# Kernel tuning notes

Hardware: AMD Instinct MI355X
Metric: run time of the kernel (lower is better)

Reference implementation:

```python
import jax, jax.numpy as jnp
import numpy as np

B, L, D, H = 2, 2048, 1024, 16
HD = D // H
SCALE = HD ** (-0.5)


def setup_inputs() -> dict:
    key = jax.random.key(0)
    ks = jax.random.split(key, 12)
    mk = lambda k, shape: (0.02 * jax.random.normal(k, shape, dtype=jnp.float32))
    return {
        "x_real": jax.random.normal(ks[0], (B, L, D), dtype=jnp.float32),
        "x_imag": jax.random.normal(ks[1], (B, L, D), dtype=jnp.float32),
        "wq_r": mk(ks[2], (D, D)),
        "wq_i": mk(ks[3], (D, D)),
        "wk_r": mk(ks[4], (D, D)),
        "wk_i": mk(ks[5], (D, D)),
        "wv_r": mk(ks[6], (D, D)),
        "wv_i": mk(ks[7], (D, D)),
        "wo_r": mk(ks[8], (D, D)),
        "wo_i": mk(ks[9], (D, D)),
        "bo_r": jnp.zeros((D,), dtype=jnp.float32),
        "bo_i": jnp.zeros((D,), dtype=jnp.float32),
    }


def _clinear(xr, xi, wr, wi):
    # (a+bi)(c+di): real = a@Wr^T - b@Wi^T ; imag = a@Wi^T + b@Wr^T
    r = xr @ wr.T - xi @ wi.T
    i = xr @ wi.T + xi @ wr.T
    return r, i


def _heads(t):
    # [B,L,D] -> [B,H,L,hd]
    return t.reshape(B, L, H, HD).transpose(0, 2, 1, 3)


def reference(x_real, x_imag, wq_r, wq_i, wk_r, wk_i, wv_r, wv_i, wo_r, wo_i, bo_r, bo_i):
    Qr, Qi = _clinear(x_real, x_imag, wq_r, wq_i)
    Kr, Ki = _clinear(x_real, x_imag, wk_r, wk_i)
    Vr, Vi = _clinear(x_real, x_imag, wv_r, wv_i)
    Qr, Qi, Kr, Ki, Vr, Vi = map(_heads, (Qr, Qi, Kr, Ki, Vr, Vi))

    # real part of complex dot product: Re(Q)Re(K)^T + Im(Q)Im(K)^T
    scores = (jnp.einsum("bhqd,bhkd->bhqk", Qr, Kr)
              + jnp.einsum("bhqd,bhkd->bhqk", Qi, Ki)) * SCALE
    causal = jnp.tril(jnp.ones((L, L), dtype=bool))
    scores = jnp.where(causal, scores, -jnp.inf)
    w = jax.nn.softmax(scores, axis=-1)

    out_r = jnp.einsum("bhqk,bhkd->bhqd", w, Vr)
    out_i = jnp.einsum("bhqk,bhkd->bhqd", w, Vi)
    merge = lambda t: t.transpose(0, 2, 1, 3).reshape(B, L, D)
    out_r, out_i = merge(out_r), merge(out_i)

    yr, yi = _clinear(out_r, out_i, wo_r, wo_i)
    return yr + bo_r, yi + bo_i
```

## Files before the change

### kernel.cpp

```cpp
#include <hip/hip_runtime.h>
#include <hip/hip_bf16.h>


using f32x4  = __attribute__((ext_vector_type(4))) float;
using short8 = __attribute__((ext_vector_type(8))) short;
using bf16_t = __hip_bfloat16;

#define AS1 __attribute__((address_space(1)))
#define AS3 __attribute__((address_space(3)))

__device__ __forceinline__ void gload_lds16(const bf16_t* g, bf16_t* l) {
  __builtin_amdgcn_global_load_lds((const AS1 unsigned int*)g, (AS3 unsigned int*)l, 16, 0, 0);
}

__device__ __forceinline__ unsigned short bfbits(float f) {
  union { bf16_t h; unsigned short u; } c; c.h = __float2bfloat16(f); return c.u;
}

__global__ void pack_x_k(const float* __restrict__ xr, const float* __restrict__ xi,
                         bf16_t* __restrict__ out) {
  const int total4 = 4096 * 2048 / 4;
  for (int idx = blockIdx.x * blockDim.x + threadIdx.x; idx < total4;
       idx += gridDim.x * blockDim.x) {
    int m = idx >> 9, k = (idx & 511) * 4;
    const float* src = (k < 1024) ? (xr + (size_t)m * 1024 + k)
                                  : (xi + (size_t)m * 1024 + (k - 1024));
    float4 v = *(const float4*)src;
    unsigned int lo = (unsigned)bfbits(v.x) | ((unsigned)bfbits(v.y) << 16);
    unsigned int hi = (unsigned)bfbits(v.z) | ((unsigned)bfbits(v.w) << 16);
    *(uint2*)(out + (size_t)idx * 4) = make_uint2(lo, hi);
  }
}

__global__ void pack_wqkv_k(const float* __restrict__ wqr, const float* __restrict__ wqi,
                            const float* __restrict__ wkr, const float* __restrict__ wki,
                            const float* __restrict__ wvr, const float* __restrict__ wvi,
                            bf16_t* __restrict__ out) {
  const int total4 = 6144 * 2048 / 4;
  for (int idx = blockIdx.x * blockDim.x + threadIdx.x; idx < total4;
       idx += gridDim.x * blockDim.x) {
    int row = idx >> 9, k = (idx & 511) * 4;
    int sec = row >> 10, r1 = row & 1023;
    bool lowk = (k < 1024);
    int kk = lowk ? k : (k - 1024);
    const float* base = wqr; float sg = 1.f;
    switch (sec) {
      case 0: base = lowk ? wqr : wqi; sg = lowk ? 1.f : -1.f; break;
      case 1: base = lowk ? wqi : wqr; break;
      case 2: base = lowk ? wkr : wki; sg = lowk ? 1.f : -1.f; break;
      case 3: base = lowk ? wki : wkr; break;
      case 4: base = lowk ? wvr : wvi; sg = lowk ? 1.f : -1.f; break;
      case 5: base = lowk ? wvi : wvr; break;
    }
    float4 v = *(const float4*)(base + (size_t)r1 * 1024 + kk);
    unsigned int lo = (unsigned)bfbits(v.x * sg) | ((unsigned)bfbits(v.y * sg) << 16);
    unsigned int hi = (unsigned)bfbits(v.z * sg) | ((unsigned)bfbits(v.w * sg) << 16);
    *(uint2*)(out + (size_t)idx * 4) = make_uint2(lo, hi);
  }
}

__global__ void pack_wo_k(const float* __restrict__ wor, const float* __restrict__ woi,
                          bf16_t* __restrict__ out) {
  const int total4 = 2048 * 2048 / 4;
  for (int idx = blockIdx.x * blockDim.x + threadIdx.x; idx < total4;
       idx += gridDim.x * blockDim.x) {
    int row = idx >> 9, k = (idx & 511) * 4;
    int sec = row >> 10, r1 = row & 1023;
    bool lowk = (k < 1024);
    int kk = lowk ? k : (k - 1024);
    const float* base; float sg = 1.f;
    if (sec == 0) { base = lowk ? wor : woi; sg = lowk ? 1.f : -1.f; }
    else          { base = lowk ? woi : wor; }
    float4 v = *(const float4*)(base + (size_t)r1 * 1024 + kk);
    unsigned int lo = (unsigned)bfbits(v.x * sg) | ((unsigned)bfbits(v.y * sg) << 16);
    unsigned int hi = (unsigned)bfbits(v.z * sg) | ((unsigned)bfbits(v.w * sg) << 16);
    *(uint2*)(out + (size_t)idx * 4) = make_uint2(lo, hi);
  }
}

__global__ __launch_bounds__(512, 2) void gemm_qkv_k(const bf16_t* __restrict__ A,
                                                     const bf16_t* __restrict__ W,
                                                     bf16_t* __restrict__ qk,
                                                     bf16_t* __restrict__ vt) {
  __shared__ __align__(16) bf16_t sA[2][256 * 64];
  __shared__ __align__(16) bf16_t sB[2][192 * 64];
  const int tid = threadIdx.x, lane = tid & 63, w = tid >> 6;
  const int wm = w >> 2, wn = w & 3;
  const int quad = lane >> 4, m16 = lane & 15;
  const int swz7 = m16 & 7;
  const int m0 = blockIdx.x * 256, n0 = blockIdx.y * 192;
  const int NT = 32;

  const int l3 = lane >> 3;
  const int gcol = (((lane & 7) ^ l3) * 8);

  f32x4 acc[8][3] = {};

  auto stageA = [&](int buf, int half, int k0) {
#pragma unroll
    for (int i = 0; i < 2; ++i)
      gload_lds16(A + (size_t)(m0 + half * 128 + w * 16 + i * 8 + l3) * 2048 + k0 + gcol,
                  &sA[buf][(size_t)(half * 128 + w * 16 + i * 8) * 64] + lane * 8);
  };
  auto stageB = [&](int buf, int c, int k0) {
    gload_lds16(W + (size_t)(n0 + c * 64 + w * 8 + l3) * 2048 + k0 + gcol,
                &sB[buf][(size_t)(c * 64 + w * 8) * 64] + lane * 8);
  };
  auto rdA = [&](const bf16_t* sAx, int mf, int kk) -> short8 {
    return *(const short8*)(sAx + (wm * 128 + mf * 16 + m16) * 64 +
                            ((kk * 4 + quad) ^ swz7) * 8);
  };
  auto rdB = [&](const bf16_t* sBx, int j, int kk) -> short8 {
    return *(const short8*)(sBx + (wn * 48 + j * 16 + m16) * 64 +
                            ((kk * 4 + quad) ^ swz7) * 8);
  };

  stageA(0, 0, 0); stageA(0, 1, 0);
  stageB(0, 0, 0); stageB(0, 1, 0); stageB(0, 2, 0);
  stageA(1, 0, 64); stageA(1, 1, 64);
  stageB(1, 0, 64); stageB(1, 1, 64); stageB(1, 2, 64);
  asm volatile("s_waitcnt vmcnt(7)" ::: "memory");
  __builtin_amdgcn_s_barrier();

  short8 A0[4], A1[4], B0[3], B1[3];
#pragma unroll
  for (int i = 0; i < 4; ++i) A0[i] = rdA(sA[0], i, 0);
#pragma unroll
  for (int j = 0; j < 3; ++j) B0[j] = rdB(sB[0], j, 0);

  for (int t = 0; t < NT; ++t) {
    const int p = t & 1, q = p ^ 1;
    const bf16_t* sAp = sA[p];
    const bf16_t* sBp = sB[p];
    const bf16_t* sAq = sA[q];
    const bf16_t* sBq = sB[q];
    const bool stg = (t + 1 < NT);
    const bool stg2 = (t + 2 < NT);

#pragma unroll
    for (int i = 0; i < 4; ++i) A1[i] = rdA(sAp, 4 + i, 0);
    __builtin_amdgcn_s_setprio(1);
#pragma unroll
    for (int i = 0; i < 4; ++i)
#pragma unroll
      for (int j = 0; j < 3; ++j)
        acc[i][j] = __builtin_amdgcn_mfma_f32_16x16x32_bf16(A0[i], B0[j], acc[i][j], 0, 0, 0);
    __builtin_amdgcn_s_setprio(0);

#pragma unroll
    for (int i = 0; i < 4; ++i) A0[i] = rdA(sAp, i, 1);
#pragma unroll
    for (int j = 0; j < 3; ++j) B1[j] = rdB(sBp, j, 1);
    __builtin_amdgcn_s_setprio(1);
#pragma unroll
    for (int i = 0; i < 4; ++i)
#pragma unroll
      for (int j = 0; j < 3; ++j)
        acc[4 + i][j] = __builtin_amdgcn_mfma_f32_16x16x32_bf16(A1[i], B0[j], acc[4 + i][j], 0, 0, 0);
    __builtin_amdgcn_s_setprio(0);

#pragma unroll
    for (int i = 0; i < 4; ++i) A1[i] = rdA(sAp, 4 + i, 1);
    __builtin_amdgcn_s_setprio(1);
#pragma unroll
    for (int i = 0; i < 4; ++i)
#pragma unroll
      for (int j = 0; j < 3; ++j)
        acc[i][j] = __builtin_amdgcn_mfma_f32_16x16x32_bf16(A0[i], B1[j], acc[i][j], 0, 0, 0);
    __builtin_amdgcn_s_setprio(0);

    asm volatile("s_waitcnt vmcnt(0)" ::: "memory");
    __builtin_amdgcn_s_barrier();

    if (stg) {
#pragma unroll
      for (int i = 0; i < 4; ++i) A0[i] = rdA(sAq, i, 0);
#pragma unroll
      for (int j = 0; j < 3; ++j) B0[j] = rdB(sBq, j, 0);
    }
    if (stg2) {
      stageA(p, 0, (t + 2) * 64); stageA(p, 1, (t + 2) * 64);
      stageB(p, 0, (t + 2) * 64); stageB(p, 1, (t + 2) * 64); stageB(p, 2, (t + 2) * 64);
    }
    __builtin_amdgcn_s_setprio(1);
#pragma unroll
    for (int i = 0; i < 4; ++i)
#pragma unroll
      for (int j = 0; j < 3; ++j)
        acc[4 + i][j] = __builtin_amdgcn_mfma_f32_16x16x32_bf16(A1[i], B1[j], acc[4 + i][j], 0, 0, 0);
    __builtin_amdgcn_s_setprio(0);
  }

#pragma unroll
  for (int mf = 0; mf < 8; ++mf) {
    const int rowb = m0 + wm * 128 + mf * 16 + quad * 4;
#pragma unroll
    for (int nf = 0; nf < 3; ++nf) {
      const int col = n0 + wn * 48 + nf * 16 + m16;
      if (col < 4096) {
        const float sc = (col < 2048) ? 0.125f : 1.f;
#pragma unroll
        for (int r = 0; r < 4; ++r)
          qk[(size_t)(rowb + r) * 4096 + col] = __float2bfloat16(acc[mf][nf][r] * sc);
      } else {
        const int vcol = col - 4096;
        const int ri = vcol >> 10, dfeat = vcol & 1023;
        const int b = rowb >> 11, seq = rowb & 2047;
        const size_t vrow = (size_t)(b * 2048 + (dfeat >> 6) * 128 + ri * 64 + (dfeat & 63));
        unsigned int lo = (unsigned)bfbits(acc[mf][nf][0]) | ((unsigned)bfbits(acc[mf][nf][1]) << 16);
        unsigned int hi = (unsigned)bfbits(acc[mf][nf][2]) | ((unsigned)bfbits(acc[mf][nf][3]) << 16);
        *(uint2*)(vt + vrow * 2048 + seq) = make_uint2(lo, hi);
      }
    }
  }
}

__global__ __launch_bounds__(512, 2) void gemm_out_k(const bf16_t* __restrict__ A,
                                                     const bf16_t* __restrict__ W,
                                                     const float* __restrict__ bor,
                                                     const float* __restrict__ boi,
                                                     float* __restrict__ out) {
  __shared__ __align__(16) bf16_t sA[2][128 * 64];
  __shared__ __align__(16) bf16_t sB[2][256 * 64];
  const int tid = threadIdx.x, lane = tid & 63, w = tid >> 6;
  const int wm = w >> 2, wn = w & 3;
  const int quad = lane >> 4, m16 = lane & 15;
  const int swz7 = m16 & 7;
  const int m0 = blockIdx.x * 128, n0 = blockIdx.y * 256;
  const int NT = 32;

  const int l3 = lane >> 3;
  const int gcol = (((lane & 7) ^ l3) * 8);

  f32x4 acc[4][4] = {};

  auto stageA = [&](int buf, int k0) {
#pragma unroll
    for (int i = 0; i < 2; ++i)
      gload_lds16(A + (size_t)(m0 + w * 16 + i * 8 + l3) * 2048 + k0 + gcol,
                  &sA[buf][(size_t)(w * 16 + i * 8) * 64] + lane * 8);
  };
  auto stageB = [&](int buf, int half, int k0) {
#pragma unroll
    for (int i = 0; i < 2; ++i)
      gload_lds16(W + (size_t)(n0 + half * 128 + w * 16 + i * 8 + l3) * 2048 + k0 + gcol,
                  &sB[buf][(size_t)(half * 128 + w * 16 + i * 8) * 64] + lane * 8);
  };
  auto rdA = [&](const bf16_t* sAx, int mf, int kk) -> short8 {
    return *(const short8*)(sAx + (wm * 64 + mf * 16 + m16) * 64 +
                            ((kk * 4 + quad) ^ swz7) * 8);
  };
  auto rdB = [&](const bf16_t* sBx, int nf, int kk) -> short8 {
    return *(const short8*)(sBx + (wn * 64 + nf * 16 + m16) * 64 +
                            ((kk * 4 + quad) ^ swz7) * 8);
  };

  stageA(0, 0);
  stageB(0, 0, 0); stageB(0, 1, 0);
  stageA(1, 64);
  stageB(1, 0, 64); stageB(1, 1, 64);
  asm volatile("s_waitcnt vmcnt(6)" ::: "memory");
  __builtin_amdgcn_s_barrier();

  short8 A0[2], A1[2], B0[4], B1[4];
#pragma unroll
  for (int i = 0; i < 2; ++i) A0[i] = rdA(sA[0], i, 0);
#pragma unroll
  for (int j = 0; j < 4; ++j) B0[j] = rdB(sB[0], j, 0);

  for (int t = 0; t < NT; ++t) {
    const int p = t & 1, q = p ^ 1;
    const bf16_t* sAp = sA[p];
    const bf16_t* sBp = sB[p];
    const bf16_t* sAq = sA[q];
    const bf16_t* sBq = sB[q];
    const bool stg = (t + 1 < NT);
    const bool stg2 = (t + 2 < NT);

#pragma unroll
    for (int i = 0; i < 2; ++i) A1[i] = rdA(sAp, 2 + i, 0);
    __builtin_amdgcn_s_setprio(1);
#pragma unroll
    for (int i = 0; i < 2; ++i)
#pragma unroll
      for (int j = 0; j < 4; ++j)
        acc[i][j] = __builtin_amdgcn_mfma_f32_16x16x32_bf16(A0[i], B0[j], acc[i][j], 0, 0, 0);
    __builtin_amdgcn_s_setprio(0);

#pragma unroll
    for (int i = 0; i < 2; ++i) A0[i] = rdA(sAp, i, 1);
#pragma unroll
    for (int j = 0; j < 4; ++j) B1[j] = rdB(sBp, j, 1);
    __builtin_amdgcn_s_setprio(1);
#pragma unroll
    for (int i = 0; i < 2; ++i)
#pragma unroll
      for (int j = 0; j < 4; ++j)
        acc[2 + i][j] = __builtin_amdgcn_mfma_f32_16x16x32_bf16(A1[i], B0[j], acc[2 + i][j], 0, 0, 0);
    __builtin_amdgcn_s_setprio(0);

#pragma unroll
    for (int i = 0; i < 2; ++i) A1[i] = rdA(sAp, 2 + i, 1);
    __builtin_amdgcn_s_setprio(1);
#pragma unroll
    for (int i = 0; i < 2; ++i)
#pragma unroll
      for (int j = 0; j < 4; ++j)
        acc[i][j] = __builtin_amdgcn_mfma_f32_16x16x32_bf16(A0[i], B1[j], acc[i][j], 0, 0, 0);
    __builtin_amdgcn_s_setprio(0);

    asm volatile("s_waitcnt vmcnt(0)" ::: "memory");
    __builtin_amdgcn_s_barrier();

    if (stg) {
#pragma unroll
      for (int i = 0; i < 2; ++i) A0[i] = rdA(sAq, i, 0);
#pragma unroll
      for (int j = 0; j < 4; ++j) B0[j] = rdB(sBq, j, 0);
    }
    if (stg2) {
      stageA(p, (t + 2) * 64);
      stageB(p, 0, (t + 2) * 64); stageB(p, 1, (t + 2) * 64);
    }
    __builtin_amdgcn_s_setprio(1);
#pragma unroll
    for (int i = 0; i < 2; ++i)
#pragma unroll
      for (int j = 0; j < 4; ++j)
        acc[2 + i][j] = __builtin_amdgcn_mfma_f32_16x16x32_bf16(A1[i], B1[j], acc[2 + i][j], 0, 0, 0);
    __builtin_amdgcn_s_setprio(0);
  }

#pragma unroll
  for (int mf = 0; mf < 4; ++mf) {
    const int rowb = m0 + wm * 64 + mf * 16 + quad * 4;
#pragma unroll
    for (int nf = 0; nf < 4; ++nf) {
      const int col = n0 + wn * 64 + nf * 16 + m16;
      float bias; float* op;
      if (col < 1024) { bias = bor[col]; op = out + col; }
      else            { bias = boi[col - 1024]; op = out + 4194304 + (col - 1024); }
#pragma unroll
      for (int r = 0; r < 4; ++r)
        op[(size_t)(rowb + r) * 1024] = acc[mf][nf][r] + bias;
    }
  }
}

__global__ __launch_bounds__(512, 4) void attn_k(const bf16_t* __restrict__ qk,
                                                 const bf16_t* __restrict__ vt,
                                                 bf16_t* __restrict__ acat) {
  __shared__ __align__(16) bf16_t sK[64 * 128];
  __shared__ __align__(16) bf16_t sV[144 * 64];
  __shared__ __align__(16) bf16_t sP[8][16 * 72];
  const int tid = threadIdx.x, lane = tid & 63, w = tid >> 6;
  const int wq = w & 3, sub = w >> 2;
  const int quad = lane >> 4, m16 = lane & 15;
  const int bx = blockIdx.x;
  const int x = (bx & 1) ? (15 - (bx >> 1)) : (bx >> 1);
  const int bh = blockIdx.y, b = bh >> 4, h = bh & 15;
  const size_t qkrow0 = (size_t)b * 2048;
  const int qA = x * 64, qB = (31 - x) * 64;
  const int nT = 32 - x;
  const int swz7 = m16 & 7;
  const int qbase = (sub ? qB : qA) + wq * 16;

  if (tid < 256) {
    const int rr = tid >> 4, cb = (tid & 15) * 4;
    const bf16_t v = __float2bfloat16(rr == 0 ? 1.f : 0.f);
#pragma unroll
    for (int i = 0; i < 4; ++i) sV[(128 + rr) * 64 + cb + i] = v;
  }

  short8 qf[4];
  {
    const bf16_t* qa = qk + (qkrow0 + qbase + m16) * 4096;
#pragma unroll
    for (int kk = 0; kk < 4; ++kk) {
      const int col = (kk >> 1) * 1024 + h * 64 + (kk & 1) * 32 + quad * 8;
      qf[kk] = *(const short8*)(qa + col);
    }
  }
  f32x4 o[9];
#pragma unroll
  for (int j = 0; j < 9; ++j) o[j] = (f32x4){0.f, 0.f, 0.f, 0.f};

  const int qrow = qbase + quad * 4;

  const int kl4 = lane >> 4, kl15 = lane & 15;
  const int vl3 = lane >> 3;
  const int vg7 = ((lane & 7) ^ vl3) * 8;

  for (int t = 0; t < nT; ++t) {
    const int k0 = t * 64;
    __syncthreads();
#pragma unroll
    for (int i = 0; i < 2; ++i) {
      const int row = w * 8 + i * 4 + kl4;
      const int g = kl15 ^ (row & 7);
      const int col = 2048 + (g >> 3) * 1024 + h * 64 + (g & 7) * 8;
      gload_lds16(qk + (qkrow0 + k0 + row) * 4096 + col,
                  sK + (size_t)(w * 8 + i * 4) * 128 + lane * 8);
    }
#pragma unroll
    for (int i = 0; i < 2; ++i) {
      const int row = w * 16 + i * 8 + vl3;
      gload_lds16(vt + ((size_t)bh * 128 + row) * 2048 + k0 + vg7,
                  sV + (size_t)(w * 16 + i * 8) * 64 + lane * 8);
    }
    __syncthreads();

    const bool act = sub ? true : (t <= x);
    if (act) {
      const bool dg = sub ? (t == nT - 1) : (t == x);

      f32x4 sv[4];
#pragma unroll
      for (int jt = 0; jt < 4; ++jt) {
        f32x4 a = (f32x4){0.f, 0.f, 0.f, 0.f};
#pragma unroll
        for (int kk = 0; kk < 4; ++kk) {
          short8 kf = *(const short8*)(sK + (jt * 16 + m16) * 128 +
                                       ((kk * 4 + quad) ^ swz7) * 8);
          a = __builtin_amdgcn_mfma_f32_16x16x32_bf16(qf[kk], kf, a, 0, 0, 0);
        }
        sv[jt] = a;
      }

      bf16_t* pw = sP[w];
#pragma unroll
      for (int jt = 0; jt < 4; ++jt)
#pragma unroll
        for (int r = 0; r < 4; ++r) {
          float s = sv[jt][r];
          if (dg && (k0 + jt * 16 + m16 > qrow + r)) s = -1e30f;
          pw[(quad * 4 + r) * 72 + jt * 16 + m16] = __float2bfloat16(__expf(s));
        }
      asm volatile("s_waitcnt lgkmcnt(0)" ::: "memory");

#pragma unroll
      for (int kc = 0; kc < 2; ++kc) {
        short8 p = *(const short8*)(pw + m16 * 72 + kc * 32 + quad * 8);
#pragma unroll
        for (int j = 0; j < 9; ++j) {
          short8 vf = *(const short8*)(sV + (j * 16 + m16) * 64 +
                                       ((kc * 4 + quad) ^ swz7) * 8);
          o[j] = __builtin_amdgcn_mfma_f32_16x16x32_bf16(p, vf, o[j], 0, 0, 0);
        }
      }
    }
  }

  float inv[4];
#pragma unroll
  for (int r = 0; r < 4; ++r)
    inv[r] = 1.f / __shfl(o[8][r], lane & 48);
#pragma unroll
  for (int j = 0; j < 8; ++j) {
    const int d = j * 16 + m16;
    const int col = (d < 64) ? (h * 64 + d) : (1024 + h * 64 + (d - 64));
#pragma unroll
    for (int r = 0; r < 4; ++r)
      acat[((size_t)b * 2048 + qrow + r) * 2048 + col] = __float2bfloat16(o[j][r] * inv[r]);
  }
}

extern "C" void kernel_launch(void* const* d_in, const int* in_sizes, int n_in,
                              void* d_out, int out_size, void* d_ws, size_t ws_size,
                              hipStream_t stream) {
  const float* xr  = (const float*)d_in[0];
  const float* xi  = (const float*)d_in[1];
  const float* wqr = (const float*)d_in[2];
  const float* wqi = (const float*)d_in[3];
  const float* wkr = (const float*)d_in[4];
  const float* wki = (const float*)d_in[5];
  const float* wvr = (const float*)d_in[6];
  const float* wvi = (const float*)d_in[7];
  const float* wor = (const float*)d_in[8];
  const float* woi = (const float*)d_in[9];
  const float* bor = (const float*)d_in[10];
  const float* boi = (const float*)d_in[11];
  float* out = (float*)d_out;

  char* ws = (char*)d_ws;
  bf16_t* Xcat = (bf16_t*)(ws);
  bf16_t* Wqkv = (bf16_t*)(ws + 16777216ull);
  bf16_t* QKb  = (bf16_t*)(ws + 41943040ull);
  bf16_t* Vt   = (bf16_t*)(ws + 75497472ull);
  bf16_t* Acat = (bf16_t*)(ws + 92274688ull);
  bf16_t* Wo   = (bf16_t*)(ws + 109051904ull);

  pack_x_k<<<2048, 256, 0, stream>>>(xr, xi, Xcat);
  pack_wqkv_k<<<2048, 256, 0, stream>>>(wqr, wqi, wkr, wki, wvr, wvi, Wqkv);
  pack_wo_k<<<1024, 256, 0, stream>>>(wor, woi, Wo);
  gemm_qkv_k<<<dim3(16, 32), 512, 0, stream>>>(Xcat, Wqkv, QKb, Vt);
  attn_k<<<dim3(16, 32), 512, 0, stream>>>(QKb, Vt, Acat);
  gemm_out_k<<<dim3(32, 8), 512, 0, stream>>>(Acat, Wo, bor, boi, out);
}
```

Before: 338.8 us.

## Widen QKV GEMM tile to 256x384 with BK=32 and simpler pipeline

Reshapes the QKV projection GEMM block tile from 256x192 with a K-step of 64 to 256x384 with a K-step of 32. Each wave now accumulates an 8x6 fragment grid instead of 8x3, which doubles B-operand reuse per A load and halves the grid to 256 blocks. The register-level software pipeline is simplified to load all fragments, then issue MFMAs split around the barrier. The LDS swizzle changes to match 32-wide rows. Costs are higher accumulator register pressure under launch_bounds(512,2), fewer blocks to fill the CUs, and twice as many barrier iterations.

Result: slower. 384.8 us (+13.6%).

```diff
diff --git a/kernel.cpp b/kernel.cpp
--- a/kernel.cpp
+++ b/kernel.cpp
@@ -82,112 +82,76 @@
                                                      const bf16_t* __restrict__ W,
                                                      bf16_t* __restrict__ qk,
                                                      bf16_t* __restrict__ vt) {
-  __shared__ __align__(16) bf16_t sA[2][256 * 64];
-  __shared__ __align__(16) bf16_t sB[2][192 * 64];
+  __shared__ __align__(16) bf16_t sA[2][256 * 32];
+  __shared__ __align__(16) bf16_t sB[2][384 * 32];
   const int tid = threadIdx.x, lane = tid & 63, w = tid >> 6;
   const int wm = w >> 2, wn = w & 3;
   const int quad = lane >> 4, m16 = lane & 15;
-  const int swz7 = m16 & 7;
-  const int m0 = blockIdx.x * 256, n0 = blockIdx.y * 192;
-  const int NT = 32;
-
-  const int l3 = lane >> 3;
-  const int gcol = (((lane & 7) ^ l3) * 8);
-
-  f32x4 acc[8][3] = {};
-
-  auto stageA = [&](int buf, int half, int k0) {
-#pragma unroll
-    for (int i = 0; i < 2; ++i)
-      gload_lds16(A + (size_t)(m0 + half * 128 + w * 16 + i * 8 + l3) * 2048 + k0 + gcol,
-                  &sA[buf][(size_t)(half * 128 + w * 16 + i * 8) * 64] + lane * 8);
-  };
-  auto stageB = [&](int buf, int c, int k0) {
-    gload_lds16(W + (size_t)(n0 + c * 64 + w * 8 + l3) * 2048 + k0 + gcol,
-                &sB[buf][(size_t)(c * 64 + w * 8) * 64] + lane * 8);
-  };
-  auto rdA = [&](const bf16_t* sAx, int mf, int kk) -> short8 {
-    return *(const short8*)(sAx + (wm * 128 + mf * 16 + m16) * 64 +
-                            ((kk * 4 + quad) ^ swz7) * 8);
-  };
-  auto rdB = [&](const bf16_t* sBx, int j, int kk) -> short8 {
-    return *(const short8*)(sBx + (wn * 48 + j * 16 + m16) * 64 +
-                            ((kk * 4 + quad) ^ swz7) * 8);
-  };
-
-  stageA(0, 0, 0); stageA(0, 1, 0);
-  stageB(0, 0, 0); stageB(0, 1, 0); stageB(0, 2, 0);
-  stageA(1, 0, 64); stageA(1, 1, 64);
-  stageB(1, 0, 64); stageB(1, 1, 64); stageB(1, 2, 64);
-  asm volatile("s_waitcnt vmcnt(7)" ::: "memory");
+  const int sw2 = (m16 >> 1) & 3;
+  const int m0 = blockIdx.x * 256, n0 = blockIdx.y * 384;
+  const int NT = 64;
+
+  const int l2 = lane >> 2;
+  const int ga = (((lane & 3) ^ ((lane >> 3) & 3)) * 8);
+
+  f32x4 acc[8][6] = {};
+
+  auto stageA = [&](int buf, int k0) {
+#pragma unroll
+    for (int i = 0; i < 2; ++i) {
+      const int R0 = w * 32 + i * 16;
+      gload_lds16(A + (size_t)(m0 + R0 + l2) * 2048 + k0 + ga,
+                  &sA[buf][(size_t)R0 * 32] + lane * 8);
+    }
+  };
+  auto stageB = [&](int buf, int k0) {
+#pragma unroll
+    for (int i = 0; i < 3; ++i) {
+      const int R0 = w * 48 + i * 16;
+      gload_lds16(W + (size_t)(n0 + R0 + l2) * 2048 + k0 + ga,
+                  &sB[buf][(size_t)R0 * 32] + lane * 8);
+    }
+  };
+  auto rdA = [&](const bf16_t* sAx, int mf) -> short8 {
+    return *(const short8*)(sAx + (wm * 128 + mf * 16 + m16) * 32 + (quad ^ sw2) * 8);
+  };
+  auto rdB = [&](const bf16_t* sBx, int nf) -> short8 {
+    return *(const short8*)(sBx + (wn * 96 + nf * 16 + m16) * 32 + (quad ^ sw2) * 8);
+  };
+
+  stageA(0, 0); stageB(0, 0);
+  stageA(1, 32); stageB(1, 32);
+  asm volatile("s_waitcnt vmcnt(5)" ::: "memory");
   __builtin_amdgcn_s_barrier();
 
-  short8 A0[4], A1[4], B0[3], B1[3];
-#pragma unroll
-  for (int i = 0; i < 4; ++i) A0[i] = rdA(sA[0], i, 0);
-#pragma unroll
-  for (int j = 0; j < 3; ++j) B0[j] = rdB(sB[0], j, 0);
-
   for (int t = 0; t < NT; ++t) {
-    const int p = t & 1, q = p ^ 1;
-    const bf16_t* sAp = sA[p];
-    const bf16_t* sBp = sB[p];
-    const bf16_t* sAq = sA[q];
-    const bf16_t* sBq = sB[q];
-    const bool stg = (t + 1 < NT);
-    const bool stg2 = (t + 2 < NT);
-
-#pragma unroll
-    for (int i = 0; i < 4; ++i) A1[i] = rdA(sAp, 4 + i, 0);
-    __builtin_amdgcn_s_setprio(1);
-#pragma unroll
-    for (int i = 0; i < 4; ++i)
-#pragma unroll
-      for (int j = 0; j < 3; ++j)
-        acc[i][j] = __builtin_amdgcn_mfma_f32_16x16x32_bf16(A0[i], B0[j], acc[i][j], 0, 0, 0);
-    __builtin_amdgcn_s_setprio(0);
-
-#pragma unroll
-    for (int i = 0; i < 4; ++i) A0[i] = rdA(sAp, i, 1);
-#pragma unroll
-    for (int j = 0; j < 3; ++j) B1[j] = rdB(sBp, j, 1);
-    __builtin_amdgcn_s_setprio(1);
-#pragma unroll
-    for (int i = 0; i < 4; ++i)
-#pragma unroll
-      for (int j = 0; j < 3; ++j)
-        acc[4 + i][j] = __builtin_amdgcn_mfma_f32_16x16x32_bf16(A1[i], B0[j], acc[4 + i][j], 0, 0, 0);
-    __builtin_amdgcn_s_setprio(0);
-
-#pragma unroll
-    for (int i = 0; i < 4; ++i) A1[i] = rdA(sAp, 4 + i, 1);
-    __builtin_amdgcn_s_setprio(1);
-#pragma unroll
-    for (int i = 0; i < 4; ++i)
-#pragma unroll
-      for (int j = 0; j < 3; ++j)
-        acc[i][j] = __builtin_amdgcn_mfma_f32_16x16x32_bf16(A0[i], B1[j], acc[i][j], 0, 0, 0);
+    const int cur = t & 1;
+    const bf16_t* sAc = sA[cur];
+    const bf16_t* sBc = sB[cur];
+
+    short8 Af[8], Bf[6];
+#pragma unroll
+    for (int mf = 0; mf < 8; ++mf) Af[mf] = rdA(sAc, mf);
+#pragma unroll
+    for (int nf = 0; nf < 6; ++nf) Bf[nf] = rdB(sBc, nf);
+    __builtin_amdgcn_s_setprio(1);
+#pragma unroll
+    for (int nf = 0; nf < 3; ++nf)
+#pragma unroll
+      for (int mf = 0; mf < 8; ++mf)
+        acc[mf][nf] = __builtin_amdgcn_mfma_f32_16x16x32_bf16(Af[mf], Bf[nf], acc[mf][nf], 0, 0, 0);
     __builtin_amdgcn_s_setprio(0);
 
     asm volatile("s_waitcnt vmcnt(0)" ::: "memory");
     __builtin_amdgcn_s_barrier();
 
-    if (stg) {
-#pragma unroll
-      for (int i = 0; i < 4; ++i) A0[i] = rdA(sAq, i, 0);
-#pragma unroll
-      for (int j = 0; j < 3; ++j) B0[j] = rdB(sBq, j, 0);
-    }
-    if (stg2) {
-      stageA(p, 0, (t + 2) * 64); stageA(p, 1, (t + 2) * 64);
-      stageB(p, 0, (t + 2) * 64); stageB(p, 1, (t + 2) * 64); stageB(p, 2, (t + 2) * 64);
-    }
-    __builtin_amdgcn_s_setprio(1);
-#pragma unroll
-    for (int i = 0; i < 4; ++i)
-#pragma unroll
-      for (int j = 0; j < 3; ++j)
-        acc[4 + i][j] = __builtin_amdgcn_mfma_f32_16x16x32_bf16(A1[i], B1[j], acc[4 + i][j], 0, 0, 0);
+    if (t + 2 < NT) { stageA(cur, (t + 2) * 32); stageB(cur, (t + 2) * 32); }
+    __builtin_amdgcn_s_setprio(1);
+#pragma unroll
+    for (int nf = 3; nf < 6; ++nf)
+#pragma unroll
+      for (int mf = 0; mf < 8; ++mf)
+        acc[mf][nf] = __builtin_amdgcn_mfma_f32_16x16x32_bf16(Af[mf], Bf[nf], acc[mf][nf], 0, 0, 0);
     __builtin_amdgcn_s_setprio(0);
   }
 
@@ -195,8 +159,8 @@
   for (int mf = 0; mf < 8; ++mf) {
     const int rowb = m0 + wm * 128 + mf * 16 + quad * 4;
 #pragma unroll
-    for (int nf = 0; nf < 3; ++nf) {
-      const int col = n0 + wn * 48 + nf * 16 + m16;
+    for (int nf = 0; nf < 6; ++nf) {
+      const int col = n0 + wn * 96 + nf * 16 + m16;
       if (col < 4096) {
         const float sc = (col < 2048) ? 0.125f : 1.f;
 #pragma unroll
@@ -493,7 +457,7 @@
   pack_x_k<<<2048, 256, 0, stream>>>(xr, xi, Xcat);
   pack_wqkv_k<<<2048, 256, 0, stream>>>(wqr, wqi, wkr, wki, wvr, wvi, Wqkv);
   pack_wo_k<<<1024, 256, 0, stream>>>(wor, woi, Wo);
-  gemm_qkv_k<<<dim3(16, 32), 512, 0, stream>>>(Xcat, Wqkv, QKb, Vt);
+  gemm_qkv_k<<<dim3(16, 16), 512, 0, stream>>>(Xcat, Wqkv, QKb, Vt);
   attn_k<<<dim3(16, 32), 512, 0, stream>>>(QKb, Vt, Acat);
   gemm_out_k<<<dim3(32, 8), 512, 0, stream>>>(Acat, Wo, bor, boi, out);
 }
```
